# Optimization experiments

Measured on AMD Instinct MI355X. Metric: run time of the kernel, lower is better.

Reference implementation:

```python
import jax, jax.numpy as jnp
import numpy as np

B, Q_LEN, HIDDEN, N_HEADS, HEAD_DIM = 8, 256, 4096, 32, 128
BLOCK_SIZE, BLOCKS_PER_SEQ, NUM_BLOCKS = 64, 12, 96
MAX_HIST = 512
ROPE_BASE = 10000.0


def setup_inputs() -> dict:
    key = jax.random.key(0)
    ks = jax.random.split(key, 8)
    hidden_states = jax.random.normal(ks[0], (1, B * Q_LEN, HIDDEN), jnp.float32)
    c_attn_w = jax.random.normal(ks[1], (3 * HIDDEN, HIDDEN), jnp.float32) * 0.02
    c_attn_b = jax.random.normal(ks[2], (3 * HIDDEN,), jnp.float32) * 0.02
    c_proj_w = jax.random.normal(ks[3], (HIDDEN, HIDDEN), jnp.float32) * 0.02
    k_cache = jax.random.normal(ks[4], (NUM_BLOCKS, BLOCK_SIZE, N_HEADS, HEAD_DIM), jnp.float32)
    v_cache = jax.random.normal(ks[5], (NUM_BLOCKS, BLOCK_SIZE, N_HEADS, HEAD_DIM), jnp.float32)
    history_lengths = jax.random.randint(ks[6], (B,), 0, MAX_HIST)
    block_offsets = jnp.arange(B * BLOCKS_PER_SEQ, dtype=jnp.int32).reshape(B, BLOCKS_PER_SEQ)
    return dict(hidden_states=hidden_states, c_attn_w=c_attn_w, c_attn_b=c_attn_b,
                c_proj_w=c_proj_w, k_cache=k_cache, v_cache=v_cache,
                history_lengths=history_lengths, block_offsets=block_offsets)


def _rotate_half(x):
    x1, x2 = x[..., :HEAD_DIM // 2], x[..., HEAD_DIM // 2:]
    return jnp.concatenate([-x2, x1], axis=-1)


def reference(hidden_states, c_attn_w, c_attn_b, c_proj_w, k_cache, v_cache,
              history_lengths, block_offsets):
    T = B * Q_LEN  # total tokens (continuous batching, flattened)
    x = hidden_states[0]  # [T, HIDDEN]
    # fused QKV projection
    qkv = x @ c_attn_w.T + c_attn_b  # [T, 3*HIDDEN]
    q, k, v = jnp.split(qkv, 3, axis=-1)
    q = q.reshape(T, N_HEADS, HEAD_DIM)
    k = k.reshape(T, N_HEADS, HEAD_DIM)
    v = v.reshape(T, N_HEADS, HEAD_DIM)
    # per-token absolute positions (position_ids_1d)
    positions = (history_lengths[:, None] + jnp.arange(Q_LEN)).reshape(-1)  # [T]
    # RoPE (ntk_alpha = 1)
    inv_freq = 1.0 / (ROPE_BASE ** (jnp.arange(0, HEAD_DIM, 2, dtype=jnp.float32) / HEAD_DIM))
    freqs = positions.astype(jnp.float32)[:, None] * inv_freq  # [T, D/2]
    emb = jnp.concatenate([freqs, freqs], axis=-1)  # [T, D]
    cos, sin = jnp.cos(emb)[:, None, :], jnp.sin(emb)[:, None, :]

    def rope(t):
        tf = t.astype(jnp.float32)
        return (tf * cos + _rotate_half(tf) * sin).astype(t.dtype)

    q, k = rope(q), rope(k)
    # fill_kv_cache: scatter new K/V into paged blocks at slot = position
    seq_ids = jnp.repeat(jnp.arange(B), Q_LEN)  # [T]
    blk = block_offsets[seq_ids, positions // BLOCK_SIZE]  # [T]
    slot = positions % BLOCK_SIZE  # [T]
    k_cache = k_cache.at[blk, slot].set(k)
    v_cache = v_cache.at[blk, slot].set(v)
    # paged attention: gather each sequence's blocks -> [B, KV, H, D]
    KV = BLOCKS_PER_SEQ * BLOCK_SIZE
    keys = k_cache[block_offsets].reshape(B, KV, N_HEADS, HEAD_DIM)
    vals = v_cache[block_offsets].reshape(B, KV, N_HEADS, HEAD_DIM)
    q_b = q.reshape(B, Q_LEN, N_HEADS, HEAD_DIM)
    scale = 1.0 / jnp.sqrt(jnp.asarray(HEAD_DIM, jnp.float32))
    scores = jnp.einsum('bqhd,bkhd->bhqk', q_b, keys) * scale  # [B,H,Q,KV]
    q_global = history_lengths[:, None] + jnp.arange(Q_LEN)  # [B,Q]
    causal = jnp.arange(KV)[None, None, :] <= q_global[:, :, None]  # [B,Q,KV]
    scores = jnp.where(causal[:, None, :, :], scores, jnp.finfo(scores.dtype).min)
    probs = jax.nn.softmax(scores, axis=-1)
    attn = jnp.einsum('bhqk,bkhd->bqhd', probs, vals).reshape(T, HIDDEN)
    out = attn @ c_proj_w.T  # c_proj (bias-free)
    return out.reshape(1, T, HIDDEN)
```

## Files before the change

kernel.cpp:

```cpp
#include <hip/hip_runtime.h>

typedef unsigned short ushort_t;
typedef float f32x4 __attribute__((ext_vector_type(4)));
typedef _Float16 f16x8 __attribute__((ext_vector_type(8)));
typedef short s16x8 __attribute__((ext_vector_type(8)));

#define NB 8
#define QL 256
#define HID 4096
#define NH 32
#define HD 128

__device__ __forceinline__ _Float16 f2h(float f) { return (_Float16)f; }
__device__ __forceinline__ ushort_t h2u(_Float16 h) {
  union { _Float16 h; ushort_t u; } x; x.h = h; return x.u;
}
__device__ __forceinline__ float u2f(ushort_t u) {
  union { _Float16 h; ushort_t u; } x; x.u = u; return (float)x.h;
}

#define MFMA16H(a, b, c) __builtin_amdgcn_mfma_f32_16x16x32_f16((a), (b), (c), 0, 0, 0)
#define AS1 __attribute__((address_space(1)))
#define AS3 __attribute__((address_space(3)))

__global__ __launch_bounds__(256)
void conv_tile(const float* __restrict__ src, ushort_t* __restrict__ dst,
               int K, int ntiles) {
  const int tile = blockIdx.x * 4 + (threadIdx.x >> 6);
  if (tile >= ntiles) return;
  const int u = threadIdx.x & 63;
  const int row = u >> 2, seg = u & 3;
  const int K32 = K >> 5;
  const int mb = tile / K32, kb = tile % K32;
  const float* sp = src + (size_t)(mb * 16 + row) * K + kb * 32 + seg * 8;
  ushort_t t[8];
#pragma unroll
  for (int j = 0; j < 8; ++j) t[j] = h2u(f2h(sp[j]));
  *(s16x8*)(dst + (size_t)tile * 512 + (((seg << 4) | row) * 8)) = *(s16x8*)t;
}

__global__ __launch_bounds__(256)
void retile_h(const ushort_t* __restrict__ src, ushort_t* __restrict__ dst,
              int K, int ntiles) {
  const int tile = blockIdx.x * 4 + (threadIdx.x >> 6);
  if (tile >= ntiles) return;
  const int u = threadIdx.x & 63;
  const int row = u >> 2, seg = u & 3;
  const int K32 = K >> 5;
  const int mb = tile / K32, kb = tile % K32;
  const s16x8 v = *(const s16x8*)(src + (size_t)(mb * 16 + row) * K + kb * 32 + seg * 8);
  *(s16x8*)(dst + (size_t)tile * 512 + (((seg << 4) | row) * 8)) = v;
}

#define VM3 asm volatile("s_waitcnt vmcnt(3)" ::: "memory")
#define VM0 asm volatile("s_waitcnt vmcnt(0)" ::: "memory")
#define NOSTG

template<int ADD_BIAS, int OUT_F32, int NT>
__global__ __launch_bounds__(512, 4)
void gemm_t(const ushort_t* __restrict__ At, const ushort_t* __restrict__ Bt,
            const float* __restrict__ bias, ushort_t* __restrict__ Ch,
            float* __restrict__ Cf, int N) {
  static_assert(NT % 3 == 2 && NT >= 8, "tail assumes NT%3==2");
  extern __shared__ ushort_t lds[];
  const int nwg = gridDim.x, bid = blockIdx.x;
  const int wg = (bid & 7) * (nwg >> 3) + (bid >> 3);
  const int mi = wg & 7, ni = wg >> 3;
  const int tid = threadIdx.x, w = tid >> 6, l = tid & 63;
  const int l16 = l & 15, lg = l >> 4;
  const int wm = w >> 1, wn = w & 1;

  const ushort_t* sA0 = At + ((size_t)(mi * 16 + 2 * w) * NT) * 512 + l * 8;
  const ushort_t* sA1 = At + ((size_t)(mi * 16 + 2 * w + 1) * NT) * 512 + l * 8;
  const ushort_t* sB  = Bt + ((size_t)(ni * 8 + w) * NT) * 512 + l * 8;

  int aof[4], bof[4];
#pragma unroll
  for (int mf = 0; mf < 4; ++mf) aof[mf] = (wm * 4 + mf) * 512 + l * 8;
#pragma unroll
  for (int nf = 0; nf < 4; ++nf) bof[nf] = 8192 + (wn * 4 + nf) * 512 + l * 8;

  f32x4 acc[4][4];
#pragma unroll
  for (int m = 0; m < 4; ++m)
#pragma unroll
    for (int n = 0; n < 4; ++n) acc[m][n] = (f32x4){0.f, 0.f, 0.f, 0.f};

#define GLDS(srcp, dstofs)                                                    \
  __builtin_amdgcn_global_load_lds((const AS1 void*)(srcp),                   \
                                   (AS3 void*)&lds[dstofs], 16, 0, 0)
#define STG(R, J)                                                             \
  do {                                                                        \
    GLDS(sA0 + (size_t)(J) * 512, (R) * 12288 + (2 * w) * 512);               \
    GLDS(sA1 + (size_t)(J) * 512, (R) * 12288 + (2 * w + 1) * 512);           \
    GLDS(sB + (size_t)(J) * 512, (R) * 12288 + 8192 + w * 512);               \
  } while (0)

#define ITER(R, VMW, STGCODE)                                                 \
  do {                                                                        \
    VMW;                                                                      \
    __builtin_amdgcn_s_barrier();                                             \
    STGCODE;                                                                  \
    f16x8 fa[4], fb[4];                                                       \
    _Pragma("unroll") for (int mf = 0; mf < 4; ++mf)                          \
        fa[mf] = *(const f16x8*)&lds[(R) * 12288 + aof[mf]];                  \
    _Pragma("unroll") for (int nf = 0; nf < 4; ++nf)                          \
        fb[nf] = *(const f16x8*)&lds[(R) * 12288 + bof[nf]];                  \
    asm volatile("s_waitcnt lgkmcnt(0)" ::: "memory");                        \
    __builtin_amdgcn_sched_barrier(0);                                        \
    __builtin_amdgcn_s_setprio(1);                                            \
    _Pragma("unroll") for (int mf = 0; mf < 4; ++mf)                          \
    _Pragma("unroll") for (int nf = 0; nf < 4; ++nf)                          \
        acc[mf][nf] = MFMA16H(fa[mf], fb[nf], acc[mf][nf]);                   \
    __builtin_amdgcn_s_setprio(0);                                            \
  } while (0)

  STG(0, 0);
  STG(1, 1);
  for (int j = 0; j < NT - 2; j += 3) {
    ITER(0, VM3, STG(2, j + 2));
    ITER(1, VM3, STG(0, j + 3));
    ITER(2, VM3, STG(1, j + 4));
  }
  ITER(0, VM3, NOSTG);
  ITER(1, VM0, NOSTG);

#pragma unroll
  for (int nf = 0; nf < 4; ++nf) {
    const int col = ni * 128 + wn * 64 + nf * 16 + l16;
    const float bi = ADD_BIAS ? bias[col] : 0.f;
#pragma unroll
    for (int mf = 0; mf < 4; ++mf) {
      const int row0 = mi * 256 + wm * 64 + mf * 16 + lg * 4;
#pragma unroll
      for (int rr = 0; rr < 4; ++rr) {
        if (OUT_F32)
          Cf[(size_t)(row0 + rr) * N + col] = acc[mf][nf][rr] + bi;
        else
          Ch[(size_t)(row0 + rr) * N + col] = h2u(f2h(acc[mf][nf][rr] + bi));
      }
    }
  }
#undef GLDS
#undef STG
#undef ITER
}

__global__ __launch_bounds__(256)
void rope_split(const ushort_t* __restrict__ qkv, const int* __restrict__ hist,
                ushort_t* __restrict__ q_r, ushort_t* __restrict__ k_r,
                ushort_t* __restrict__ v_r) {
  const int t = blockIdx.x;
  const int b = t >> 8, qq = t & 255;
  __shared__ float cs[64], sn[64];
  const int tid = threadIdx.x;
  if (tid < 64) {
    const float pos = (float)(hist[b] + qq);
    const float f = pos * __expf(-(float)tid * (9.210340371976184f / 64.0f));
    cs[tid] = cosf(f);
    sn[tid] = sinf(f);
  }
  __syncthreads();
  const ushort_t* src = qkv + (size_t)t * 12288;
  const float qscale = 0.08838834764831845f;
  for (int i = tid; i < NH * 64; i += 256) {
    const int h = i >> 6, j = i & 63;
    const float c = cs[j], s = sn[j];
    const size_t dst = ((size_t)(b * NH + h) * QL + qq) * HD;
    {
      const float x1 = u2f(src[h * HD + j]);
      const float x2 = u2f(src[h * HD + j + 64]);
      q_r[dst + j]      = h2u(f2h((x1 * c - x2 * s) * qscale));
      q_r[dst + j + 64] = h2u(f2h((x2 * c + x1 * s) * qscale));
    }
    {
      const float x1 = u2f(src[HID + h * HD + j]);
      const float x2 = u2f(src[HID + h * HD + j + 64]);
      k_r[dst + j]      = h2u(f2h(x1 * c - x2 * s));
      k_r[dst + j + 64] = h2u(f2h(x2 * c + x1 * s));
    }
    v_r[dst + j]      = src[2 * HID + h * HD + j];
    v_r[dst + j + 64] = src[2 * HID + h * HD + j + 64];
  }
}

__global__ __launch_bounds__(512, 2)
void attn_fwd(const ushort_t* __restrict__ q_r, const ushort_t* __restrict__ k_r,
              const ushort_t* __restrict__ v_r,
              const float* __restrict__ k_cache, const float* __restrict__ v_cache,
              const int* __restrict__ hist, const int* __restrict__ bofs,
              ushort_t* __restrict__ attn_h) {
  const int bh = blockIdx.x;
  const int b = bh >> 5, h = bh & 31;
  const int hb = hist[b];

  __shared__ ushort_t K_lds[64 * 136];
  __shared__ ushort_t V_lds[128 * 72];
  __shared__ ushort_t P_lds[256 * 72];

  const int tid = threadIdx.x;
  const int w = tid >> 6, l = tid & 63;
  const int l16 = l & 15, lg = l >> 4;

  f16x8 qf[2][4];
#pragma unroll
  for (int m = 0; m < 2; ++m) {
    const int qrow = w * 32 + m * 16 + l16;
    const ushort_t* qp = q_r + ((size_t)(b * NH + h) * QL + qrow) * HD + lg * 8;
#pragma unroll
    for (int kd = 0; kd < 4; ++kd) qf[m][kd] = *(const f16x8*)(qp + kd * 32);
  }

  f32x4 o[2][8];
  float mr[2][4], sr[2][4];
#pragma unroll
  for (int m = 0; m < 2; ++m) {
#pragma unroll
    for (int d = 0; d < 8; ++d) o[m][d] = (f32x4){0.f, 0.f, 0.f, 0.f};
#pragma unroll
    for (int r = 0; r < 4; ++r) { mr[m][r] = -1e30f; sr[m][r] = 0.f; }
  }

  const int nt = (hb + QL + 63) >> 6;
  const int srow = tid >> 4;
  const int seg = tid & 15;

  for (int t = 0; t < nt; ++t) {
    const int kv0 = t << 6;
    __syncthreads();
#pragma unroll
    for (int p = 0; p < 2; ++p) {
      const int row = p * 32 + srow;
      const int kvg = kv0 + row;
      if (kvg < hb) {
        const int blk = bofs[b * 12 + t];
        const size_t base = ((size_t)blk * 64 + (kvg & 63)) * HID + h * HD;
        const float* kf = k_cache + base;
        const float* vf = v_cache + base;
        ushort_t tmp[8];
#pragma unroll
        for (int j = 0; j < 8; ++j) tmp[j] = h2u(f2h(kf[seg * 8 + j]));
        *(s16x8*)&K_lds[row * 136 + seg * 8] = *(s16x8*)tmp;
#pragma unroll
        for (int j = 0; j < 8; ++j) {
          const int d = seg + j * 16;
          V_lds[d * 72 + row] = h2u(f2h(vf[d]));
        }
      } else {
        int r2 = kvg - hb;
        if (r2 > QL - 1) r2 = QL - 1;
        const size_t base = ((size_t)(b * NH + h) * QL + r2) * HD;
        const ushort_t* kb = k_r + base;
        const ushort_t* vb = v_r + base;
        *(s16x8*)&K_lds[row * 136 + seg * 8] = *(const s16x8*)(kb + seg * 8);
#pragma unroll
        for (int j = 0; j < 8; ++j) {
          const int d = seg + j * 16;
          V_lds[d * 72 + row] = vb[d];
        }
      }
    }
    __syncthreads();

    f32x4 sa[2][4];
#pragma unroll
    for (int m = 0; m < 2; ++m)
#pragma unroll
      for (int n = 0; n < 4; ++n) sa[m][n] = (f32x4){0.f, 0.f, 0.f, 0.f};
#pragma unroll
    for (int kd = 0; kd < 4; ++kd) {
      f16x8 kf[4];
#pragma unroll
      for (int n = 0; n < 4; ++n)
        kf[n] = *(const f16x8*)&K_lds[(n * 16 + l16) * 136 + kd * 32 + lg * 8];
#pragma unroll
      for (int m = 0; m < 2; ++m)
#pragma unroll
        for (int n = 0; n < 4; ++n)
          sa[m][n] = MFMA16H(qf[m][kd], kf[n], sa[m][n]);
    }

#pragma unroll
    for (int m = 0; m < 2; ++m) {
#pragma unroll
      for (int n = 0; n < 4; ++n) {
        const int kvg = kv0 + n * 16 + l16;
#pragma unroll
        for (int r = 0; r < 4; ++r) {
          const int qg = hb + w * 32 + m * 16 + lg * 4 + r;
          if (kvg > qg) sa[m][n][r] = -1e30f;
        }
      }
      float tm[4], ts[4];
#pragma unroll
      for (int r = 0; r < 4; ++r)
        tm[r] = fmaxf(fmaxf(sa[m][0][r], sa[m][1][r]),
                      fmaxf(sa[m][2][r], sa[m][3][r]));
#pragma unroll
      for (int x = 1; x < 16; x <<= 1)
#pragma unroll
        for (int r = 0; r < 4; ++r)
          tm[r] = fmaxf(tm[r], __shfl_xor(tm[r], x, 16));
#pragma unroll
      for (int r = 0; r < 4; ++r) {
        const float nm = fmaxf(mr[m][r], tm[r]);
        const float corr = __expf(mr[m][r] - nm);
        mr[m][r] = nm;
        sr[m][r] *= corr;
#pragma unroll
        for (int d = 0; d < 8; ++d) o[m][d][r] *= corr;
        ts[r] = 0.f;
      }
#pragma unroll
      for (int n = 0; n < 4; ++n)
#pragma unroll
        for (int r = 0; r < 4; ++r) {
          const float p = __expf(sa[m][n][r] - mr[m][r]);
          sa[m][n][r] = p;
          ts[r] += p;
        }
#pragma unroll
      for (int x = 1; x < 16; x <<= 1)
#pragma unroll
        for (int r = 0; r < 4; ++r) ts[r] += __shfl_xor(ts[r], x, 16);
#pragma unroll
      for (int r = 0; r < 4; ++r) sr[m][r] += ts[r];
#pragma unroll
      for (int n = 0; n < 4; ++n)
#pragma unroll
        for (int r = 0; r < 4; ++r)
          P_lds[(w * 32 + m * 16 + lg * 4 + r) * 72 + n * 16 + l16] =
              h2u(f2h(sa[m][n][r]));
    }

#pragma unroll
    for (int ks = 0; ks < 2; ++ks) {
      f16x8 pa[2];
#pragma unroll
      for (int m = 0; m < 2; ++m)
        pa[m] = *(const f16x8*)&P_lds[(w * 32 + m * 16 + l16) * 72 + ks * 32 + lg * 8];
#pragma unroll
      for (int d = 0; d < 8; ++d) {
        const f16x8 vb =
            *(const f16x8*)&V_lds[(d * 16 + l16) * 72 + ks * 32 + lg * 8];
#pragma unroll
        for (int m = 0; m < 2; ++m) o[m][d] = MFMA16H(pa[m], vb, o[m][d]);
      }
    }
  }

#pragma unroll
  for (int m = 0; m < 2; ++m)
#pragma unroll
    for (int r = 0; r < 4; ++r) {
      const int qrow = w * 32 + m * 16 + lg * 4 + r;
      const float inv = 1.0f / sr[m][r];
      const size_t obase = ((size_t)(b * QL + qrow)) * HID + h * HD;
#pragma unroll
      for (int d = 0; d < 8; ++d)
        attn_h[obase + d * 16 + l16] = h2u(f2h(o[m][d][r] * inv));
    }
}

extern "C" void kernel_launch(void* const* d_in, const int* in_sizes, int n_in,
                              void* d_out, int out_size, void* d_ws,
                              size_t ws_size, hipStream_t stream) {
  const float* hidden   = (const float*)d_in[0];
  const float* c_attn_w = (const float*)d_in[1];
  const float* c_attn_b = (const float*)d_in[2];
  const float* c_proj_w = (const float*)d_in[3];
  const float* k_cache  = (const float*)d_in[4];
  const float* v_cache  = (const float*)d_in[5];
  const int* hist       = (const int*)d_in[6];
  const int* bofs       = (const int*)d_in[7];
  float* out = (float*)d_out;

  char* ws = (char*)d_ws;
  const size_t MB = 1ull << 20;
  ushort_t* w_attn_t = (ushort_t*)(ws);
  ushort_t* wproj_t  = (ushort_t*)(ws);
  ushort_t* qkv_h   = (ushort_t*)(ws + 100 * MB);
  ushort_t* attn_h  = (ushort_t*)(ws + 100 * MB);
  ushort_t* attn_t  = (ushort_t*)(ws + 116 * MB);
  ushort_t* q_r = (ushort_t*)(ws + 148 * MB);
  ushort_t* k_r = (ushort_t*)(ws + 164 * MB);
  ushort_t* v_r = (ushort_t*)(ws + 180 * MB);
  ushort_t* x_t = (ushort_t*)(ws + 196 * MB);

  conv_tile<<<4096, 256, 0, stream>>>(hidden, x_t, 4096, 16384);
  conv_tile<<<24576, 256, 0, stream>>>(c_attn_w, w_attn_t, 4096, 98304);
  gemm_t<1, 0, 128><<<768, 512, 73728, stream>>>(x_t, w_attn_t, c_attn_b,
                                                 qkv_h, nullptr, 12288);
  rope_split<<<2048, 256, 0, stream>>>(qkv_h, hist, q_r, k_r, v_r);
  conv_tile<<<8192, 256, 0, stream>>>(c_proj_w, wproj_t, 4096, 32768);
  attn_fwd<<<256, 512, 0, stream>>>(q_r, k_r, v_r, k_cache, v_cache, hist,
                                    bofs, attn_h);
  retile_h<<<4096, 256, 0, stream>>>(attn_h, attn_t, 4096, 16384);
  gemm_t<0, 1, 128><<<256, 512, 73728, stream>>>(attn_t, wproj_t, nullptr,
                                                 nullptr, out, 4096);
}
```

Before: 455.1 us.

## Apply RoPE in place on QKV and write attention output pre-tiled

RoPE is now applied in place inside the QKV buffer with vectorized 8-wide loads and stores, so the separate head-major copies of Q, K and V are no longer written. Attention reads Q/K/V directly from the strided QKV rows, and its epilogue writes output straight into the tiled layout the projection GEMM expects, which removes the retile kernel. This cuts global memory traffic and one launch. In exchange, attention reads from rows with a large stride and its final stores are scattered rather than coalesced.

```diff
diff --git a/kernel.cpp b/kernel.cpp
--- a/kernel.cpp
+++ b/kernel.cpp
@@ -37,19 +37,6 @@
 #pragma unroll
   for (int j = 0; j < 8; ++j) t[j] = h2u(f2h(sp[j]));
   *(s16x8*)(dst + (size_t)tile * 512 + (((seg << 4) | row) * 8)) = *(s16x8*)t;
-}
-
-__global__ __launch_bounds__(256)
-void retile_h(const ushort_t* __restrict__ src, ushort_t* __restrict__ dst,
-              int K, int ntiles) {
-  const int tile = blockIdx.x * 4 + (threadIdx.x >> 6);
-  if (tile >= ntiles) return;
-  const int u = threadIdx.x & 63;
-  const int row = u >> 2, seg = u & 3;
-  const int K32 = K >> 5;
-  const int mb = tile / K32, kb = tile % K32;
-  const s16x8 v = *(const s16x8*)(src + (size_t)(mb * 16 + row) * K + kb * 32 + seg * 8);
-  *(s16x8*)(dst + (size_t)tile * 512 + (((seg << 4) | row) * 8)) = v;
 }
 
 #define VM3 asm volatile("s_waitcnt vmcnt(3)" ::: "memory")
@@ -147,9 +134,7 @@
 }
 
 __global__ __launch_bounds__(256)
-void rope_split(const ushort_t* __restrict__ qkv, const int* __restrict__ hist,
-                ushort_t* __restrict__ q_r, ushort_t* __restrict__ k_r,
-                ushort_t* __restrict__ v_r) {
+void rope_inplace(ushort_t* __restrict__ qkv, const int* __restrict__ hist) {
   const int t = blockIdx.x;
   const int b = t >> 8, qq = t & 255;
   __shared__ float cs[64], sn[64];
@@ -161,35 +146,48 @@
     sn[tid] = sinf(f);
   }
   __syncthreads();
-  const ushort_t* src = qkv + (size_t)t * 12288;
+  ushort_t* row = qkv + (size_t)t * 12288;
+  const int h = tid >> 3;
+  const int j0 = (tid & 7) * 8;
   const float qscale = 0.08838834764831845f;
-  for (int i = tid; i < NH * 64; i += 256) {
-    const int h = i >> 6, j = i & 63;
-    const float c = cs[j], s = sn[j];
-    const size_t dst = ((size_t)(b * NH + h) * QL + qq) * HD;
-    {
-      const float x1 = u2f(src[h * HD + j]);
-      const float x2 = u2f(src[h * HD + j + 64]);
-      q_r[dst + j]      = h2u(f2h((x1 * c - x2 * s) * qscale));
-      q_r[dst + j + 64] = h2u(f2h((x2 * c + x1 * s) * qscale));
-    }
-    {
-      const float x1 = u2f(src[HID + h * HD + j]);
-      const float x2 = u2f(src[HID + h * HD + j + 64]);
-      k_r[dst + j]      = h2u(f2h(x1 * c - x2 * s));
-      k_r[dst + j + 64] = h2u(f2h(x2 * c + x1 * s));
-    }
-    v_r[dst + j]      = src[2 * HID + h * HD + j];
-    v_r[dst + j + 64] = src[2 * HID + h * HD + j + 64];
+  float c[8], s[8];
+#pragma unroll
+  for (int j = 0; j < 8; ++j) { c[j] = cs[j0 + j]; s[j] = sn[j0 + j]; }
+  {
+    ushort_t* p1 = row + h * HD + j0;
+    ushort_t* p2 = p1 + 64;
+    s16x8 a = *(s16x8*)p1, bb = *(s16x8*)p2;
+    ushort_t o1[8], o2[8];
+#pragma unroll
+    for (int j = 0; j < 8; ++j) {
+      const float x1 = u2f((ushort_t)a[j]), x2 = u2f((ushort_t)bb[j]);
+      o1[j] = h2u(f2h((x1 * c[j] - x2 * s[j]) * qscale));
+      o2[j] = h2u(f2h((x2 * c[j] + x1 * s[j]) * qscale));
+    }
+    *(s16x8*)p1 = *(s16x8*)o1;
+    *(s16x8*)p2 = *(s16x8*)o2;
+  }
+  {
+    ushort_t* p1 = row + HID + h * HD + j0;
+    ushort_t* p2 = p1 + 64;
+    s16x8 a = *(s16x8*)p1, bb = *(s16x8*)p2;
+    ushort_t o1[8], o2[8];
+#pragma unroll
+    for (int j = 0; j < 8; ++j) {
+      const float x1 = u2f((ushort_t)a[j]), x2 = u2f((ushort_t)bb[j]);
+      o1[j] = h2u(f2h(x1 * c[j] - x2 * s[j]));
+      o2[j] = h2u(f2h(x2 * c[j] + x1 * s[j]));
+    }
+    *(s16x8*)p1 = *(s16x8*)o1;
+    *(s16x8*)p2 = *(s16x8*)o2;
   }
 }
 
 __global__ __launch_bounds__(512, 2)
-void attn_fwd(const ushort_t* __restrict__ q_r, const ushort_t* __restrict__ k_r,
-              const ushort_t* __restrict__ v_r,
+void attn_fwd(const ushort_t* __restrict__ qkv,
               const float* __restrict__ k_cache, const float* __restrict__ v_cache,
               const int* __restrict__ hist, const int* __restrict__ bofs,
-              ushort_t* __restrict__ attn_h) {
+              ushort_t* __restrict__ attn_t) {
   const int bh = blockIdx.x;
   const int b = bh >> 5, h = bh & 31;
   const int hb = hist[b];
@@ -206,7 +204,7 @@
 #pragma unroll
   for (int m = 0; m < 2; ++m) {
     const int qrow = w * 32 + m * 16 + l16;
-    const ushort_t* qp = q_r + ((size_t)(b * NH + h) * QL + qrow) * HD + lg * 8;
+    const ushort_t* qp = qkv + (size_t)(b * QL + qrow) * 12288 + h * HD + lg * 8;
 #pragma unroll
     for (int kd = 0; kd < 4; ++kd) qf[m][kd] = *(const f16x8*)(qp + kd * 32);
   }
@@ -249,9 +247,9 @@
       } else {
         int r2 = kvg - hb;
         if (r2 > QL - 1) r2 = QL - 1;
-        const size_t base = ((size_t)(b * NH + h) * QL + r2) * HD;
-        const ushort_t* kb = k_r + base;
-        const ushort_t* vb = v_r + base;
+        const size_t base = (size_t)(b * QL + r2) * 12288 + h * HD;
+        const ushort_t* kb = qkv + base + HID;
+        const ushort_t* vb = qkv + base + 2 * HID;
         *(s16x8*)&K_lds[row * 136 + seg * 8] = *(const s16x8*)(kb + seg * 8);
 #pragma unroll
         for (int j = 0; j < 8; ++j) {
@@ -350,16 +348,20 @@
   }
 
 #pragma unroll
-  for (int m = 0; m < 2; ++m)
+  for (int m = 0; m < 2; ++m) {
+    const int rb = b * 16 + w * 2 + m;
 #pragma unroll
     for (int r = 0; r < 4; ++r) {
-      const int qrow = w * 32 + m * 16 + lg * 4 + r;
       const float inv = 1.0f / sr[m][r];
-      const size_t obase = ((size_t)(b * QL + qrow)) * HID + h * HD;
-#pragma unroll
-      for (int d = 0; d < 8; ++d)
-        attn_h[obase + d * 16 + l16] = h2u(f2h(o[m][d][r] * inv));
-    }
+#pragma unroll
+      for (int d = 0; d < 8; ++d) {
+        const int kb = h * 4 + (d >> 1);
+        const int lane_dst = (lg * 4 + r) | ((((d & 1) << 1) | (l16 >> 3)) << 4);
+        attn_t[((size_t)(rb * 128 + kb)) * 512 + lane_dst * 8 + (l16 & 7)] =
+            h2u(f2h(o[m][d][r] * inv));
+      }
+    }
+  }
 }
 
 extern "C" void kernel_launch(void* const* d_in, const int* in_sizes, int n_in,
@@ -380,22 +382,17 @@
   ushort_t* w_attn_t = (ushort_t*)(ws);
   ushort_t* wproj_t  = (ushort_t*)(ws);
   ushort_t* qkv_h   = (ushort_t*)(ws + 100 * MB);
-  ushort_t* attn_h  = (ushort_t*)(ws + 100 * MB);
-  ushort_t* attn_t  = (ushort_t*)(ws + 116 * MB);
-  ushort_t* q_r = (ushort_t*)(ws + 148 * MB);
-  ushort_t* k_r = (ushort_t*)(ws + 164 * MB);
-  ushort_t* v_r = (ushort_t*)(ws + 180 * MB);
-  ushort_t* x_t = (ushort_t*)(ws + 196 * MB);
+  ushort_t* attn_t  = (ushort_t*)(ws + 148 * MB);
+  ushort_t* x_t     = (ushort_t*)(ws + 196 * MB);
 
   conv_tile<<<4096, 256, 0, stream>>>(hidden, x_t, 4096, 16384);
   conv_tile<<<24576, 256, 0, stream>>>(c_attn_w, w_attn_t, 4096, 98304);
   gemm_t<1, 0, 128><<<768, 512, 73728, stream>>>(x_t, w_attn_t, c_attn_b,
                                                  qkv_h, nullptr, 12288);
-  rope_split<<<2048, 256, 0, stream>>>(qkv_h, hist, q_r, k_r, v_r);
+  rope_inplace<<<2048, 256, 0, stream>>>(qkv_h, hist);
   conv_tile<<<8192, 256, 0, stream>>>(c_proj_w, wproj_t, 4096, 32768);
-  attn_fwd<<<256, 512, 0, stream>>>(q_r, k_r, v_r, k_cache, v_cache, hist,
-                                    bofs, attn_h);
-  retile_h<<<4096, 256, 0, stream>>>(attn_h, attn_t, 4096, 16384);
+  attn_fwd<<<256, 512, 0, stream>>>(qkv_h, k_cache, v_cache, hist, bofs,
+                                    attn_t);
   gemm_t<0, 1, 128><<<256, 512, 73728, stream>>>(attn_t, wproj_t, nullptr,
                                                  nullptr, out, 4096);
 }
```

After: 412.0 us. 1.1x faster.
